# Optimization experiments

Hardware: AMD Instinct MI355X
Metric: run time of the kernel (lower is better)

Reference implementation:

```python
import jax, jax.numpy as jnp
import numpy as np

# Dims from GlobalFractalRouterConfig defaults
B, D, FP, H, NF, A = 65536, 512, 64, 256, 4, 32


def _norm(x):
    # F.normalize(dim=-1) with eps=1e-12
    return x / jnp.clip(jnp.linalg.norm(x, axis=-1, keepdims=True), 1e-12)


def setup_inputs() -> dict:
    key = jax.random.key(0)
    ks = jax.random.split(key, 12)
    s = 0.02
    return {
        "features": jax.random.normal(ks[0], (B, D), jnp.float32),
        "source_fingerprint": jax.random.normal(ks[1], (FP,), jnp.float32),
        "target_fingerprint": jax.random.normal(ks[2], (FP,), jnp.float32),
        # field_generators: NF stacked (Linear(D+FP,H) -> GELU -> Linear(H,1))
        "Wf1": jax.random.normal(ks[3], (NF, D + FP, H), jnp.float32) * s,
        "bf1": jnp.zeros((NF, H), jnp.float32),
        "Wf2": jax.random.normal(ks[4], (NF, H), jnp.float32) * s,
        "bf2": jnp.zeros((NF,), jnp.float32),
        # compat_proj: Linear(2*FP, NF)
        "Wc": jax.random.normal(ks[5], (2 * FP, NF), jnp.float32) * s,
        "bc": jnp.zeros((NF,), jnp.float32),
        # gate_net: Linear(2*NF+FP, H) -> GELU -> Linear(H, D) -> Sigmoid
        "Wg1": jax.random.normal(ks[6], (2 * NF + FP, H), jnp.float32) * s,
        "bg1": jnp.zeros((H,), jnp.float32),
        "Wg2": jax.random.normal(ks[7], (H, D), jnp.float32) * s,
        "bg2": jnp.zeros((D,), jnp.float32),
        # AnchorBank
        "E": jax.random.normal(ks[8], (A, D), jnp.float32) * s,  # anchor_embeddings
        "Wfp": jax.random.normal(ks[9], (D, D), jnp.float32) * s,  # feature_proj
        "bfp": jnp.zeros((D,), jnp.float32),
        "Wfq": jax.random.normal(ks[10], (FP, D), jnp.float32) * s,  # fingerprint_proj
        "bfq": jnp.zeros((D,), jnp.float32),
    }


def _potential(feats, fp_vec, Wf1, bf1, Wf2, bf2):
    # AdjacentGate.compute_potential, all fields vectorized
    b = feats.shape[0]
    comb = jnp.concatenate(
        [feats, jnp.broadcast_to(fp_vec, (b, fp_vec.shape[0]))], axis=-1
    )  # [B, D+FP]
    h = jax.nn.gelu(jnp.einsum('bi,fih->bfh', comb, Wf1) + bf1, approximate=False)
    return jnp.einsum('bfh,fh->bf', h, Wf2) + bf2  # [B, NF]


def reference(features, source_fingerprint, target_fingerprint,
              Wf1, bf1, Wf2, bf2, Wc, bc, Wg1, bg1, Wg2, bg2,
              E, Wfp, bfp, Wfq, bfq):
    b = features.shape[0]
    # --- AdjacentGate ---
    p_src = _potential(features, source_fingerprint, Wf1, bf1, Wf2, bf2)
    p_tgt = _potential(features, target_fingerprint, Wf1, bf1, Wf2, bf2)
    gradient = p_tgt - p_src  # [B, NF]
    fp_comb = jnp.concatenate([source_fingerprint, target_fingerprint])  # [2*FP]
    compat = jnp.tanh(fp_comb @ Wc + bc)  # [NF]
    gate_in = jnp.concatenate(
        [gradient,
         jnp.broadcast_to(compat, (b, compat.shape[0])),
         jnp.broadcast_to(source_fingerprint, (b, source_fingerprint.shape[0]))],
        axis=-1)  # [B, 2*NF+FP]
    gate = jax.nn.sigmoid(
        jax.nn.gelu(gate_in @ Wg1 + bg1, approximate=False) @ Wg2 + bg2)  # [B, D]
    gated = features * gate
    # --- AnchorBank ---
    feat_proj = _norm(gated @ Wfp + bfp)  # [B, D]
    anchors_norm = _norm(E)  # [A, D]
    aff = feat_proj @ anchors_norm.T  # [B, A]
    fp_proj = source_fingerprint @ Wfq + bfq  # [D]
    aff = aff + 0.3 * (anchors_norm @ fp_proj)
    aff = jax.nn.softmax(aff, axis=-1)
    anchor_features = aff @ E  # [B, D]
    return gated + anchor_features
```

## Files before the change

### kernel.cpp

```cpp
#include <hip/hip_runtime.h>
#include <hip/hip_bf16.h>

typedef unsigned short u16;
typedef __attribute__((ext_vector_type(8))) __bf16 bf16x8;
typedef __attribute__((ext_vector_type(8))) short  s16x8;
typedef __attribute__((ext_vector_type(4))) short  s16x4;
typedef __attribute__((ext_vector_type(4))) float  f32x4;

#define NB 65536
#define OFF_GRAD   0u
#define OFF_SUMSQ  1048576u
#define OFF_CONSTS 1310720u
#define OFF_WF1T   1327104u
#define OFF_WG2T   2375680u
#define OFF_WFPT   2637824u
#define OFF_ET     3162112u
#define OFF_AFF    3194880u
#define OFF_GATED  7389184u
#define WS_NEEDED  74498048u
#define CI_SRC   0
#define CI_TGT   1024
#define CI_C0    2048
#define CI_INVE  2304
#define CI_ABIAS 2336

__device__ inline float bf2f(u16 u) { union { unsigned int i; float f; } v; v.i = ((unsigned int)u) << 16; return v.f; }
__device__ inline u16 f2bf(float f) { union { float f; unsigned int i; } v; v.f = f; return (u16)((v.i + 0x7fffu + ((v.i >> 16) & 1u)) >> 16); }
__device__ inline float gelu(float x) {
  float z = 1.5957691216f * x * (1.0f + 0.044715f * x * x);
  return x * __builtin_amdgcn_rcpf(1.0f + __expf(-z));
}
__device__ inline float sigm(float x) { return __builtin_amdgcn_rcpf(1.0f + __expf(-x)); }

typedef __attribute__((address_space(3))) unsigned int as3_u32;
typedef __attribute__((address_space(1))) unsigned int as1_u32;
__device__ __forceinline__ void gload16(const u16* g, u16* l) {
  __builtin_amdgcn_global_load_lds((const as1_u32*)g, (as3_u32*)l, 16, 0, 0);
}

__global__ __launch_bounds__(256) void k_cvt(const float* __restrict__ feat, u16* __restrict__ featbf) {
  int idx = (blockIdx.x << 8) + threadIdx.x;
  const float4* src = (const float4*)feat + (idx << 1);
  float4 v0 = src[0], v1 = src[1];
  s16x8 o;
  o[0] = (short)f2bf(v0.x); o[1] = (short)f2bf(v0.y);
  o[2] = (short)f2bf(v0.z); o[3] = (short)f2bf(v0.w);
  o[4] = (short)f2bf(v1.x); o[5] = (short)f2bf(v1.y);
  o[6] = (short)f2bf(v1.z); o[7] = (short)f2bf(v1.w);
  *(s16x8*)(featbf + (idx << 3)) = o;
}

__global__ __launch_bounds__(256) void k_pre(
    const float* __restrict__ sfp, const float* __restrict__ tfp,
    const float* __restrict__ wf1, const float* __restrict__ bf1,
    const float* __restrict__ wc,  const float* __restrict__ bc,
    const float* __restrict__ wg1, const float* __restrict__ bg1,
    const float* __restrict__ wfq, const float* __restrict__ bfq,
    const float* __restrict__ E,   float* __restrict__ consts)
{
  __shared__ float s_s[64], s_t[64], s_c[4], s_fp[512];
  const int t = threadIdx.x;
  const int b = blockIdx.x;
  if (t < 64) { s_s[t] = sfp[t]; s_t[t] = tfp[t]; }
  __syncthreads();
  if (b < 8) {
    if (t < 128) {
      int n = b * 128 + t;
      int f = n >> 8, h = n & 255;
      float as = bf1[f * 256 + h];
      float at = as;
      const float* col = wf1 + f * 147456 + 512 * 256 + h;
      #pragma unroll 8
      for (int j = 0; j < 64; ++j) {
        float wv = col[j * 256];
        as += s_s[j] * wv; at += s_t[j] * wv;
      }
      consts[CI_SRC + n] = as;
      consts[CI_TGT + n] = at;
    }
  } else if (b == 8) {
    if (t < 4) {
      float a = bc[t];
      for (int j = 0; j < 64; ++j)
        a += s_s[j] * wc[j * 4 + t] + s_t[j] * wc[(64 + j) * 4 + t];
      s_c[t] = tanhf(a);
    }
    __syncthreads();
    float a = bg1[t];
    #pragma unroll
    for (int f = 0; f < 4; ++f) a += s_c[f] * wg1[(4 + f) * 256 + t];
    for (int j = 0; j < 64; ++j) a += s_s[j] * wg1[(8 + j) * 256 + t];
    consts[CI_C0 + t] = a;
  } else {
    for (int d = t; d < 512; d += 256) {
      float a = bfq[d];
      for (int j = 0; j < 64; ++j) a += s_s[j] * wfq[j * 512 + d];
      s_fp[d] = a;
    }
    __syncthreads();
    if (t < 32) {
      float ss = 0.f, dot = 0.f;
      for (int d = 0; d < 512; ++d) {
        float e = E[t * 512 + d];
        ss += e * e; dot += e * s_fp[d];
      }
      float inv = 1.0f / fmaxf(sqrtf(ss), 1e-12f);
      consts[CI_INVE + t] = inv;
      consts[CI_ABIAS + t] = 0.3f * inv * dot;
    }
  }
}

__global__ __launch_bounds__(256) void k_transpose(
    const float* __restrict__ wf1, const float* __restrict__ wg2,
    const float* __restrict__ wfp, const float* __restrict__ E,
    u16* __restrict__ ws16)
{
  int tile = blockIdx.x;
  const float* src; u16* dst; int K, N, tl;
  if (tile < 512)      { int f = tile >> 7; tl = tile & 127; src = wf1 + f * 147456; dst = ws16 + (OFF_WF1T >> 1) + f * 131072; K = 512; N = 256; }
  else if (tile < 640) { tl = tile - 512; src = wg2; dst = ws16 + (OFF_WG2T >> 1); K = 256; N = 512; }
  else if (tile < 896) { tl = tile - 640; src = wfp; dst = ws16 + (OFF_WFPT >> 1); K = 512; N = 512; }
  else                 { tl = tile - 896; src = E;   dst = ws16 + (OFF_ET   >> 1); K = 32;  N = 512; }
  int ntn = N >> 5;
  int r0 = (tl / ntn) << 5, c0 = (tl % ntn) << 5;
  __shared__ float T[32][33];
  const int t = threadIdx.x;
  {
    int r = t >> 3, c4 = (t & 7) << 2;
    float4 v = *(const float4*)(src + (r0 + r) * N + c0 + c4);
    T[r][c4] = v.x; T[r][c4 + 1] = v.y; T[r][c4 + 2] = v.z; T[r][c4 + 3] = v.w;
  }
  __syncthreads();
  {
    int c = t >> 3, r4 = (t & 7) << 2;
    s16x4 v;
    v[0] = (short)f2bf(T[r4 + 0][c]); v[1] = (short)f2bf(T[r4 + 1][c]);
    v[2] = (short)f2bf(T[r4 + 2][c]); v[3] = (short)f2bf(T[r4 + 3][c]);
    *(s16x4*)(dst + (c0 + c) * K + r0 + r4) = v;
  }
}

__global__ __launch_bounds__(256, 2) void k_potential(
    const u16* __restrict__ featbf, const u16* __restrict__ wf1t,
    const float* __restrict__ wf2,  const float* __restrict__ consts,
    float* __restrict__ grad)
{
  __shared__ u16 Al[128][32];
  __shared__ u16 Bl[256][32];
  const int col0 = blockIdx.x << 8;
  const int row0 = blockIdx.y << 7;
  const int f = blockIdx.x;
  const int t = threadIdx.x;
  const int w = t >> 6, lane = t & 63, lr = lane & 15, lq = lane >> 4;
  const int gr = lane >> 2, gc = (lane & 3) << 3;

  f32x4 acc[2][16];
  #pragma unroll
  for (int i = 0; i < 2; ++i)
    #pragma unroll
    for (int j = 0; j < 16; ++j) { f32x4 z = {0.f, 0.f, 0.f, 0.f}; acc[i][j] = z; }

  for (int k0 = 0; k0 < 512; k0 += 32) {
    __syncthreads();
    #pragma unroll
    for (int j = 0; j < 2; ++j) {
      int rb = (j << 6) + (w << 4);
      gload16(featbf + (row0 + rb + gr) * 512 + k0 + gc, &Al[rb][0]);
    }
    #pragma unroll
    for (int j = 0; j < 4; ++j) {
      int rb = (j << 6) + (w << 4);
      gload16(wf1t + (col0 + rb + gr) * 512 + k0 + gc, &Bl[rb][0]);
    }
    __syncthreads();
    bf16x8 a[2];
    #pragma unroll
    for (int rt = 0; rt < 2; ++rt)
      a[rt] = *(const bf16x8*)&Al[(w << 5) + (rt << 4) + lr][lq << 3];
    #pragma unroll
    for (int ct = 0; ct < 16; ++ct) {
      bf16x8 bb = *(const bf16x8*)&Bl[(ct << 4) + lr][lq << 3];
      acc[0][ct] = __builtin_amdgcn_mfma_f32_16x16x32_bf16(a[0], bb, acc[0][ct], 0, 0, 0);
      acc[1][ct] = __builtin_amdgcn_mfma_f32_16x16x32_bf16(a[1], bb, acc[1][ct], 0, 0, 0);
    }
  }
  float part[2][4] = {{0, 0, 0, 0}, {0, 0, 0, 0}};
  #pragma unroll
  for (int ct = 0; ct < 16; ++ct) {
    int n = col0 + (ct << 4) + lr;
    float so = consts[CI_SRC + n];
    float to = consts[CI_TGT + n];
    float w2 = wf2[n];
    #pragma unroll
    for (int rt = 0; rt < 2; ++rt)
      #pragma unroll
      for (int j = 0; j < 4; ++j) {
        float c = acc[rt][ct][j];
        part[rt][j] += (gelu(c + to) - gelu(c + so)) * w2;
      }
  }
  #pragma unroll
  for (int m = 1; m <= 8; m <<= 1)
    #pragma unroll
    for (int rt = 0; rt < 2; ++rt)
      #pragma unroll
      for (int j = 0; j < 4; ++j)
        part[rt][j] += __shfl_xor(part[rt][j], m, 64);
  if (lr == 0) {
    #pragma unroll
    for (int rt = 0; rt < 2; ++rt)
      #pragma unroll
      for (int j = 0; j < 4; ++j) {
        int r = row0 + (w << 5) + (rt << 4) + (lq << 2) + j;
        grad[r * 4 + f] = part[rt][j];
      }
  }
}

__global__ __launch_bounds__(256, 2) void k_gate(
    const u16* __restrict__ featbf, const float* __restrict__ grad,
    const float* __restrict__ wg1,  const u16* __restrict__ wg2t,
    const float* __restrict__ bg2,  const float* __restrict__ consts,
    u16* __restrict__ gated)
{
  __shared__ u16 Hl[128][264];
  __shared__ u16 Bl[128][32];
  const int col0 = blockIdx.x << 7;
  const int row0 = blockIdx.y << 7;
  const int t = threadIdx.x;
  const int w = t >> 6, lane = t & 63, lr = lane & 15, lq = lane >> 4;
  const int gr = lane >> 2, gc = (lane & 3) << 3;

  {
    float wv[4], c0v = consts[CI_C0 + t];
    #pragma unroll
    for (int f = 0; f < 4; ++f) wv[f] = wg1[f * 256 + t];
    for (int i = 0; i < 128; ++i) {
      float4 g = *(const float4*)(grad + ((row0 + i) << 2));
      float p = c0v + g.x * wv[0] + g.y * wv[1] + g.z * wv[2] + g.w * wv[3];
      Hl[i][t] = f2bf(gelu(p));
    }
  }
  f32x4 acc[2][8];
  #pragma unroll
  for (int i = 0; i < 2; ++i)
    #pragma unroll
    for (int j = 0; j < 8; ++j) { f32x4 z = {0.f, 0.f, 0.f, 0.f}; acc[i][j] = z; }

  for (int k0 = 0; k0 < 256; k0 += 32) {
    __syncthreads();
    #pragma unroll
    for (int j = 0; j < 2; ++j) {
      int rb = (j << 6) + (w << 4);
      gload16(wg2t + (col0 + rb + gr) * 256 + k0 + gc, &Bl[rb][0]);
    }
    __syncthreads();
    bf16x8 a[2];
    #pragma unroll
    for (int rt = 0; rt < 2; ++rt)
      a[rt] = *(const bf16x8*)&Hl[(w << 5) + (rt << 4) + lr][k0 + (lq << 3)];
    #pragma unroll
    for (int ct = 0; ct < 8; ++ct) {
      bf16x8 bb = *(const bf16x8*)&Bl[(ct << 4) + lr][lq << 3];
      acc[0][ct] = __builtin_amdgcn_mfma_f32_16x16x32_bf16(a[0], bb, acc[0][ct], 0, 0, 0);
      acc[1][ct] = __builtin_amdgcn_mfma_f32_16x16x32_bf16(a[1], bb, acc[1][ct], 0, 0, 0);
    }
  }
  __syncthreads();
  u16* Gl = &Hl[0][0];
  #pragma unroll
  for (int ct = 0; ct < 8; ++ct) {
    int n = col0 + (ct << 4) + lr;
    float bv = bg2[n];
    #pragma unroll
    for (int rt = 0; rt < 2; ++rt)
      #pragma unroll
      for (int j = 0; j < 4; ++j) {
        int r = (w << 5) + (rt << 4) + (lq << 2) + j;
        Gl[r * 136 + (ct << 4) + lr] = f2bf(sigm(acc[rt][ct][j] + bv));
      }
  }
  __syncthreads();
  #pragma unroll
  for (int it = 0; it < 8; ++it) {
    int s = (it << 8) + t;
    int r = s >> 4, c8 = (s & 15) << 3;
    s16x8 f8 = *(const s16x8*)(featbf + (row0 + r) * 512 + col0 + c8);
    s16x8 g8 = *(const s16x8*)(Gl + r * 136 + c8);
    s16x8 o;
    #pragma unroll
    for (int j = 0; j < 8; ++j)
      o[j] = (short)f2bf(bf2f((u16)f8[j]) * bf2f((u16)g8[j]));
    *(s16x8*)(gated + (row0 + r) * 512 + col0 + c8) = o;
  }
}

__global__ __launch_bounds__(256, 2) void k_proj(
    const u16* __restrict__ gated, const u16* __restrict__ wfpt,
    const float* __restrict__ bfp, u16* __restrict__ y,
    float* __restrict__ sumsq)
{
  __shared__ u16 U[128 * 264];
  u16 (*Al)[32] = (u16(*)[32])U;
  u16 (*Bl)[32] = (u16(*)[32])(U + 4096);
  const int col0 = blockIdx.x << 8;
  const int row0 = blockIdx.y << 7;
  const int t = threadIdx.x;
  const int w = t >> 6, lane = t & 63, lr = lane & 15, lq = lane >> 4;
  const int gr = lane >> 2, gc = (lane & 3) << 3;

  f32x4 acc[2][16];
  #pragma unroll
  for (int i = 0; i < 2; ++i)
    #pragma unroll
    for (int j = 0; j < 16; ++j) { f32x4 z = {0.f, 0.f, 0.f, 0.f}; acc[i][j] = z; }

  for (int k0 = 0; k0 < 512; k0 += 32) {
    __syncthreads();
    #pragma unroll
    for (int j = 0; j < 2; ++j) {
      int rb = (j << 6) + (w << 4);
      gload16(gated + (row0 + rb + gr) * 512 + k0 + gc, &Al[rb][0]);
    }
    #pragma unroll
    for (int j = 0; j < 4; ++j) {
      int rb = (j << 6) + (w << 4);
      gload16(wfpt + (col0 + rb + gr) * 512 + k0 + gc, &Bl[rb][0]);
    }
    __syncthreads();
    bf16x8 a[2];
    #pragma unroll
    for (int rt = 0; rt < 2; ++rt)
      a[rt] = *(const bf16x8*)&Al[(w << 5) + (rt << 4) + lr][lq << 3];
    #pragma unroll
    for (int ct = 0; ct < 16; ++ct) {
      bf16x8 bb = *(const bf16x8*)&Bl[(ct << 4) + lr][lq << 3];
      acc[0][ct] = __builtin_amdgcn_mfma_f32_16x16x32_bf16(a[0], bb, acc[0][ct], 0, 0, 0);
      acc[1][ct] = __builtin_amdgcn_mfma_f32_16x16x32_bf16(a[1], bb, acc[1][ct], 0, 0, 0);
    }
  }
  float part[2][4] = {{0, 0, 0, 0}, {0, 0, 0, 0}};
  #pragma unroll
  for (int ct = 0; ct < 16; ++ct) {
    float bv = bfp[col0 + (ct << 4) + lr];
    #pragma unroll
    for (int rt = 0; rt < 2; ++rt)
      #pragma unroll
      for (int j = 0; j < 4; ++j) {
        acc[rt][ct][j] += bv;
        part[rt][j] += acc[rt][ct][j] * acc[rt][ct][j];
      }
  }
  #pragma unroll
  for (int m = 1; m <= 8; m <<= 1)
    #pragma unroll
    for (int rt = 0; rt < 2; ++rt)
      #pragma unroll
      for (int j = 0; j < 4; ++j)
        part[rt][j] += __shfl_xor(part[rt][j], m, 64);
  if (lr == 0) {
    #pragma unroll
    for (int rt = 0; rt < 2; ++rt)
      #pragma unroll
      for (int j = 0; j < 4; ++j)
        atomicAdd(&sumsq[row0 + (w << 5) + (rt << 4) + (lq << 2) + j], part[rt][j]);
  }
  __syncthreads();
  u16* Yl = U;
  #pragma unroll
  for (int ct = 0; ct < 16; ++ct)
    #pragma unroll
    for (int rt = 0; rt < 2; ++rt)
      #pragma unroll
      for (int j = 0; j < 4; ++j) {
        int r = (w << 5) + (rt << 4) + (lq << 2) + j;
        Yl[r * 264 + (ct << 4) + lr] = f2bf(acc[rt][ct][j]);
      }
  __syncthreads();
  #pragma unroll
  for (int it = 0; it < 16; ++it) {
    int s = (it << 8) + t;
    int r = s >> 5, c8 = (s & 31) << 3;
    *(s16x8*)(y + (row0 + r) * 512 + col0 + c8) = *(const s16x8*)(Yl + r * 264 + c8);
  }
}

__global__ __launch_bounds__(256, 2) void k_aff(
    const u16* __restrict__ y, const float* __restrict__ E,
    const float* __restrict__ sumsq, const float* __restrict__ consts,
    u16* __restrict__ aff)
{
  __shared__ u16 El[32][520];
  __shared__ u16 Al[256][32];
  const int row0 = blockIdx.x << 8;
  const int t = threadIdx.x;
  const int w = t >> 6, lane = t & 63, lr = lane & 15, lq = lane >> 4;
  const int gr = lane >> 2, gc = (lane & 3) << 3;
  #pragma unroll
  for (int i = 0; i < 16; ++i) {
    int s = (i << 8) + t;
    int a = s >> 7, c4 = (s & 127) << 2;
    float4 v = *(const float4*)(E + a * 512 + c4);
    s16x4 b;
    b[0] = (short)f2bf(v.x); b[1] = (short)f2bf(v.y);
    b[2] = (short)f2bf(v.z); b[3] = (short)f2bf(v.w);
    *(s16x4*)&El[a][c4] = b;
  }
  f32x4 acc[4][2];
  #pragma unroll
  for (int i = 0; i < 4; ++i)
    #pragma unroll
    for (int j = 0; j < 2; ++j) { f32x4 z = {0.f, 0.f, 0.f, 0.f}; acc[i][j] = z; }

  for (int k0 = 0; k0 < 512; k0 += 32) {
    __syncthreads();
    #pragma unroll
    for (int j = 0; j < 4; ++j) {
      int rb = (j << 6) + (w << 4);
      gload16(y + (row0 + rb + gr) * 512 + k0 + gc, &Al[rb][0]);
    }
    __syncthreads();
    bf16x8 b0 = *(const bf16x8*)&El[lr][k0 + (lq << 3)];
    bf16x8 b1 = *(const bf16x8*)&El[16 + lr][k0 + (lq << 3)];
    #pragma unroll
    for (int rt = 0; rt < 4; ++rt) {
      bf16x8 a = *(const bf16x8*)&Al[(w << 6) + (rt << 4) + lr][lq << 3];
      acc[rt][0] = __builtin_amdgcn_mfma_f32_16x16x32_bf16(a, b0, acc[rt][0], 0, 0, 0);
      acc[rt][1] = __builtin_amdgcn_mfma_f32_16x16x32_bf16(a, b1, acc[rt][1], 0, 0, 0);
    }
  }
  float iv0 = consts[CI_INVE + lr],  iv1 = consts[CI_INVE + 16 + lr];
  float ab0 = consts[CI_ABIAS + lr], ab1 = consts[CI_ABIAS + 16 + lr];
  #pragma unroll
  for (int rt = 0; rt < 4; ++rt) {
    #pragma unroll
    for (int j = 0; j < 4; ++j) {
      int r = row0 + (w << 6) + (rt << 4) + (lq << 2) + j;
      float invn = 1.0f / fmaxf(sqrtf(sumsq[r]), 1e-12f);
      float v0 = acc[rt][0][j] * iv0 * invn + ab0;
      float v1 = acc[rt][1][j] * iv1 * invn + ab1;
      float mx = fmaxf(v0, v1);
      #pragma unroll
      for (int m = 1; m <= 8; m <<= 1) mx = fmaxf(mx, __shfl_xor(mx, m, 64));
      float e0 = __expf(v0 - mx), e1 = __expf(v1 - mx);
      float sm = e0 + e1;
      #pragma unroll
      for (int m = 1; m <= 8; m <<= 1) sm += __shfl_xor(sm, m, 64);
      float rs = 1.0f / sm;
      aff[r * 32 + lr]      = f2bf(e0 * rs);
      aff[r * 32 + 16 + lr] = f2bf(e1 * rs);
    }
  }
}

__global__ __launch_bounds__(256, 2) void k_out(
    const u16* __restrict__ gated, const u16* __restrict__ aff,
    const u16* __restrict__ et, float* __restrict__ out)
{
  __shared__ u16 ETl[512][40];
  __shared__ u16 Afl[64][40];
  __shared__ u16 Ol[64][520];
  const int row0 = blockIdx.x << 6;
  const int t = threadIdx.x;
  const int w = t >> 6, lane = t & 63, lr = lane & 15, lq = lane >> 4;
  {
    int r = t >> 2, k8 = (t & 3) << 3;
    *(bf16x8*)&Afl[r][k8] = *(const bf16x8*)(aff + (row0 + r) * 32 + k8);
  }
  #pragma unroll
  for (int i = 0; i < 8; ++i) {
    int s = (i << 8) + t;
    int d = s >> 2, k8 = (s & 3) << 3;
    *(bf16x8*)&ETl[d][k8] = *(const bf16x8*)(et + d * 32 + k8);
  }
  __syncthreads();
  bf16x8 a[4];
  #pragma unroll
  for (int rt = 0; rt < 4; ++rt)
    a[rt] = *(const bf16x8*)&Afl[(rt << 4) + lr][lq << 3];
  f32x4 z = {0.f, 0.f, 0.f, 0.f};
  #pragma unroll
  for (int ct = 0; ct < 8; ++ct) {
    bf16x8 bb = *(const bf16x8*)&ETl[(w << 7) + (ct << 4) + lr][lq << 3];
    #pragma unroll
    for (int rt = 0; rt < 4; ++rt) {
      f32x4 o = __builtin_amdgcn_mfma_f32_16x16x32_bf16(a[rt], bb, z, 0, 0, 0);
      #pragma unroll
      for (int j = 0; j < 4; ++j)
        Ol[(rt << 4) + (lq << 2) + j][(w << 7) + (ct << 4) + lr] = f2bf(o[j]);
    }
  }
  __syncthreads();
  #pragma unroll
  for (int it = 0; it < 32; ++it) {
    int s = (it << 8) + t;
    int r = s >> 7, c4 = (s & 127) << 2;
    s16x4 g4 = *(const s16x4*)(gated + (row0 + r) * 512 + c4);
    s16x4 a4 = *(const s16x4*)(&Ol[0][0] + r * 520 + c4);
    float4 o;
    o.x = bf2f((u16)g4[0]) + bf2f((u16)a4[0]);
    o.y = bf2f((u16)g4[1]) + bf2f((u16)a4[1]);
    o.z = bf2f((u16)g4[2]) + bf2f((u16)a4[2]);
    o.w = bf2f((u16)g4[3]) + bf2f((u16)a4[3]);
    *(float4*)(out + (row0 + r) * 512 + c4) = o;
  }
}

extern "C" void kernel_launch(void* const* d_in, const int* in_sizes, int n_in,
                              void* d_out, int out_size, void* d_ws, size_t ws_size,
                              hipStream_t stream) {
  (void)in_sizes; (void)n_in; (void)out_size;
  if (ws_size < WS_NEEDED) return;
  const float* feat = (const float*)d_in[0];
  const float* sfp  = (const float*)d_in[1];
  const float* tfp  = (const float*)d_in[2];
  const float* wf1  = (const float*)d_in[3];
  const float* bf1  = (const float*)d_in[4];
  const float* wf2  = (const float*)d_in[5];
  const float* wc   = (const float*)d_in[7];
  const float* bc   = (const float*)d_in[8];
  const float* wg1  = (const float*)d_in[9];
  const float* bg1  = (const float*)d_in[10];
  const float* wg2  = (const float*)d_in[11];
  const float* bg2  = (const float*)d_in[12];
  const float* E    = (const float*)d_in[13];
  const float* wfp  = (const float*)d_in[14];
  const float* bfp  = (const float*)d_in[15];
  const float* wfq  = (const float*)d_in[16];
  const float* bfq  = (const float*)d_in[17];

  char* ws = (char*)d_ws;
  float* grad   = (float*)(ws + OFF_GRAD);
  float* sumsq  = (float*)(ws + OFF_SUMSQ);
  float* consts = (float*)(ws + OFF_CONSTS);
  u16* ws16  = (u16*)ws;
  u16* wf1t  = (u16*)(ws + OFF_WF1T);
  u16* wg2t  = (u16*)(ws + OFF_WG2T);
  u16* wfpt  = (u16*)(ws + OFF_WFPT);
  u16* et    = (u16*)(ws + OFF_ET);
  u16* aff   = (u16*)(ws + OFF_AFF);
  u16* gated = (u16*)(ws + OFF_GATED);
  u16* yscr  = (u16*)d_out;
  u16* featbf = (u16*)d_out + 33554432;
  float* out = (float*)d_out;

  hipMemsetAsync(ws + OFF_SUMSQ, 0, 262144, stream);
  k_cvt<<<dim3(16384), dim3(256), 0, stream>>>(feat, featbf);
  k_pre<<<dim3(10), dim3(256), 0, stream>>>(sfp, tfp, wf1, bf1, wc, bc, wg1, bg1, wfq, bfq, E, consts);
  k_transpose<<<dim3(912), dim3(256), 0, stream>>>(wf1, wg2, wfp, E, ws16);
  k_potential<<<dim3(4, 512), dim3(256), 0, stream>>>(featbf, wf1t, wf2, consts, grad);
  k_gate<<<dim3(4, 512), dim3(256), 0, stream>>>(featbf, grad, wg1, wg2t, bg2, consts, gated);
  k_proj<<<dim3(2, 512), dim3(256), 0, stream>>>(gated, wfpt, bfp, yscr, sumsq);
  k_aff<<<dim3(256), dim3(256), 0, stream>>>(yscr, E, sumsq, consts, aff);
  k_out<<<dim3(1024), dim3(256), 0, stream>>>(gated, aff, et, out);
}
```

Before: 645.6 us.

## Double-buffer LDS tiles, XOR-swizzle LDS layout, and remap block order in GEMM kernels

Converts the K-loops of the potential, gate, projection and affinity kernels to double-buffered LDS staging, so the next tile's global loads are issued while the current tile is consumed by MFMA. This halves the barriers per K-step. It also applies an XOR swizzle to LDS columns to reduce bank conflicts on the bf16x8 reads. The 2D grids are flattened to 1D with a remapped block order that interleaves blocks, likely for better cache and XCD locality. The cost is extra LDS per block, which may reduce occupancy, plus more complex indexing.

Result: no change. 635.8 us (-1.5%).

```diff
diff --git a/kernel.cpp b/kernel.cpp
--- a/kernel.cpp
+++ b/kernel.cpp
@@ -146,14 +146,18 @@
     const float* __restrict__ wf2,  const float* __restrict__ consts,
     float* __restrict__ grad)
 {
-  __shared__ u16 Al[128][32];
-  __shared__ u16 Bl[256][32];
-  const int col0 = blockIdx.x << 8;
-  const int row0 = blockIdx.y << 7;
-  const int f = blockIdx.x;
+  __shared__ u16 Al[2][128][32];
+  __shared__ u16 Bl[2][256][32];
+  const int wg = blockIdx.x;
+  const int s  = ((wg & 7) << 8) + (wg >> 3);
+  const int f  = s & 3;
+  const int col0 = f << 8;
+  const int row0 = (s >> 2) << 7;
   const int t = threadIdx.x;
   const int w = t >> 6, lane = t & 63, lr = lane & 15, lq = lane >> 4;
-  const int gr = lane >> 2, gc = (lane & 3) << 3;
+  const int gr  = lane >> 2;
+  const int gcs = ((lane & 3) ^ ((lane >> 3) & 3)) << 3;
+  const int ca  = (lq ^ ((lr >> 1) & 3)) << 3;
 
   f32x4 acc[2][16];
   #pragma unroll
@@ -161,30 +165,33 @@
     #pragma unroll
     for (int j = 0; j < 16; ++j) { f32x4 z = {0.f, 0.f, 0.f, 0.f}; acc[i][j] = z; }
 
-  for (int k0 = 0; k0 < 512; k0 += 32) {
-    __syncthreads();
-    #pragma unroll
-    for (int j = 0; j < 2; ++j) {
-      int rb = (j << 6) + (w << 4);
-      gload16(featbf + (row0 + rb + gr) * 512 + k0 + gc, &Al[rb][0]);
-    }
-    #pragma unroll
-    for (int j = 0; j < 4; ++j) {
-      int rb = (j << 6) + (w << 4);
-      gload16(wf1t + (col0 + rb + gr) * 512 + k0 + gc, &Bl[rb][0]);
-    }
-    __syncthreads();
-    bf16x8 a[2];
-    #pragma unroll
-    for (int rt = 0; rt < 2; ++rt)
-      a[rt] = *(const bf16x8*)&Al[(w << 5) + (rt << 4) + lr][lq << 3];
-    #pragma unroll
-    for (int ct = 0; ct < 16; ++ct) {
-      bf16x8 bb = *(const bf16x8*)&Bl[(ct << 4) + lr][lq << 3];
-      acc[0][ct] = __builtin_amdgcn_mfma_f32_16x16x32_bf16(a[0], bb, acc[0][ct], 0, 0, 0);
-      acc[1][ct] = __builtin_amdgcn_mfma_f32_16x16x32_bf16(a[1], bb, acc[1][ct], 0, 0, 0);
-    }
-  }
+#define STAGE_P(buf, k0) { \
+    _Pragma("unroll") for (int j = 0; j < 2; ++j) { int rb = (j << 6) + (w << 4); \
+      gload16(featbf + (row0 + rb + gr) * 512 + (k0) + gcs, &Al[buf][rb][0]); } \
+    _Pragma("unroll") for (int j = 0; j < 4; ++j) { int rb = (j << 6) + (w << 4); \
+      gload16(wf1t + (col0 + rb + gr) * 512 + (k0) + gcs, &Bl[buf][rb][0]); } }
+
+#define COMP_P(buf) { bf16x8 a[2]; \
+    _Pragma("unroll") for (int rt = 0; rt < 2; ++rt) \
+      a[rt] = *(const bf16x8*)&Al[buf][(w << 5) + (rt << 4) + lr][ca]; \
+    _Pragma("unroll") for (int ct = 0; ct < 16; ++ct) { \
+      bf16x8 bb = *(const bf16x8*)&Bl[buf][(ct << 4) + lr][ca]; \
+      acc[0][ct] = __builtin_amdgcn_mfma_f32_16x16x32_bf16(a[0], bb, acc[0][ct], 0, 0, 0); \
+      acc[1][ct] = __builtin_amdgcn_mfma_f32_16x16x32_bf16(a[1], bb, acc[1][ct], 0, 0, 0); } }
+
+  STAGE_P(0, 0);
+  __syncthreads();
+  #pragma unroll
+  for (int k0 = 0; k0 < 512; k0 += 64) {
+    STAGE_P(1, k0 + 32);
+    COMP_P(0);
+    __syncthreads();
+    if (k0 + 64 < 512) STAGE_P(0, k0 + 64);
+    COMP_P(1);
+    __syncthreads();
+  }
+#undef STAGE_P
+#undef COMP_P
   float part[2][4] = {{0, 0, 0, 0}, {0, 0, 0, 0}};
   #pragma unroll
   for (int ct = 0; ct < 16; ++ct) {
@@ -224,22 +231,33 @@
     const float* __restrict__ bg2,  const float* __restrict__ consts,
     u16* __restrict__ gated)
 {
-  __shared__ u16 Hl[128][264];
-  __shared__ u16 Bl[128][32];
-  const int col0 = blockIdx.x << 7;
-  const int row0 = blockIdx.y << 7;
+  __shared__ u16 Hl[32768];
+  __shared__ u16 Bl[2][128][32];
+  const int wg = blockIdx.x;
+  const int s  = ((wg & 7) << 8) + (wg >> 3);
+  const int col0 = (s & 3) << 7;
+  const int row0 = (s >> 2) << 7;
   const int t = threadIdx.x;
   const int w = t >> 6, lane = t & 63, lr = lane & 15, lq = lane >> 4;
-  const int gr = lane >> 2, gc = (lane & 3) << 3;
+  const int gr  = lane >> 2;
+  const int gcs = ((lane & 3) ^ ((lane >> 3) & 3)) << 3;
+  const int ca  = (lq ^ ((lr >> 1) & 3)) << 3;
+
+#define STAGE_G(buf, k0) { \
+    _Pragma("unroll") for (int j = 0; j < 2; ++j) { int rb = (j << 6) + (w << 4); \
+      gload16(wg2t + (col0 + rb + gr) * 256 + (k0) + gcs, &Bl[buf][rb][0]); } }
+
+  STAGE_G(0, 0);
 
   {
     float wv[4], c0v = consts[CI_C0 + t];
+    const int tc = t >> 3, tw = t & 7;
     #pragma unroll
     for (int f = 0; f < 4; ++f) wv[f] = wg1[f * 256 + t];
     for (int i = 0; i < 128; ++i) {
       float4 g = *(const float4*)(grad + ((row0 + i) << 2));
       float p = c0v + g.x * wv[0] + g.y * wv[1] + g.z * wv[2] + g.w * wv[3];
-      Hl[i][t] = f2bf(gelu(p));
+      Hl[i * 256 + ((tc ^ ((i >> 1) & 7)) << 3) + tw] = f2bf(gelu(p));
     }
   }
   f32x4 acc[2][8];
@@ -248,27 +266,29 @@
     #pragma unroll
     for (int j = 0; j < 8; ++j) { f32x4 z = {0.f, 0.f, 0.f, 0.f}; acc[i][j] = z; }
 
-  for (int k0 = 0; k0 < 256; k0 += 32) {
-    __syncthreads();
-    #pragma unroll
-    for (int j = 0; j < 2; ++j) {
-      int rb = (j << 6) + (w << 4);
-      gload16(wg2t + (col0 + rb + gr) * 256 + k0 + gc, &Bl[rb][0]);
-    }
-    __syncthreads();
-    bf16x8 a[2];
-    #pragma unroll
-    for (int rt = 0; rt < 2; ++rt)
-      a[rt] = *(const bf16x8*)&Hl[(w << 5) + (rt << 4) + lr][k0 + (lq << 3)];
-    #pragma unroll
-    for (int ct = 0; ct < 8; ++ct) {
-      bf16x8 bb = *(const bf16x8*)&Bl[(ct << 4) + lr][lq << 3];
-      acc[0][ct] = __builtin_amdgcn_mfma_f32_16x16x32_bf16(a[0], bb, acc[0][ct], 0, 0, 0);
-      acc[1][ct] = __builtin_amdgcn_mfma_f32_16x16x32_bf16(a[1], bb, acc[1][ct], 0, 0, 0);
-    }
-  }
-  __syncthreads();
-  u16* Gl = &Hl[0][0];
+#define COMP_G(buf, k0) { bf16x8 a[2]; \
+    _Pragma("unroll") for (int rt = 0; rt < 2; ++rt) { \
+      int r = (w << 5) + (rt << 4) + lr; \
+      int cq = (((k0) >> 3) + lq) ^ (lr >> 1); \
+      a[rt] = *(const bf16x8*)&Hl[r * 256 + (cq << 3)]; } \
+    _Pragma("unroll") for (int ct = 0; ct < 8; ++ct) { \
+      bf16x8 bb = *(const bf16x8*)&Bl[buf][(ct << 4) + lr][ca]; \
+      acc[0][ct] = __builtin_amdgcn_mfma_f32_16x16x32_bf16(a[0], bb, acc[0][ct], 0, 0, 0); \
+      acc[1][ct] = __builtin_amdgcn_mfma_f32_16x16x32_bf16(a[1], bb, acc[1][ct], 0, 0, 0); } }
+
+  __syncthreads();
+  #pragma unroll
+  for (int k0 = 0; k0 < 256; k0 += 64) {
+    STAGE_G(1, k0 + 32);
+    COMP_G(0, k0);
+    __syncthreads();
+    if (k0 + 64 < 256) STAGE_G(0, k0 + 64);
+    COMP_G(1, k0 + 32);
+    __syncthreads();
+  }
+#undef STAGE_G
+#undef COMP_G
+  u16* Gl = Hl;
   #pragma unroll
   for (int ct = 0; ct < 8; ++ct) {
     int n = col0 + (ct << 4) + lr;
@@ -284,8 +304,8 @@
   __syncthreads();
   #pragma unroll
   for (int it = 0; it < 8; ++it) {
-    int s = (it << 8) + t;
-    int r = s >> 4, c8 = (s & 15) << 3;
+    int s2 = (it << 8) + t;
+    int r = s2 >> 4, c8 = (s2 & 15) << 3;
     s16x8 f8 = *(const s16x8*)(featbf + (row0 + r) * 512 + col0 + c8);
     s16x8 g8 = *(const s16x8*)(Gl + r * 136 + c8);
     s16x8 o;
@@ -301,14 +321,20 @@
     const float* __restrict__ bfp, u16* __restrict__ y,
     float* __restrict__ sumsq)
 {
-  __shared__ u16 U[128 * 264];
-  u16 (*Al)[32] = (u16(*)[32])U;
-  u16 (*Bl)[32] = (u16(*)[32])(U + 4096);
-  const int col0 = blockIdx.x << 8;
-  const int row0 = blockIdx.y << 7;
+  __shared__ u16 U[33792];
+  u16* A0 = U;
+  u16* B0 = U + 4096;
+  u16* A1 = U + 12288;
+  u16* B1 = U + 16384;
+  const int wg = blockIdx.x;
+  const int s  = ((wg & 7) << 7) + (wg >> 3);
+  const int col0 = (s & 1) << 8;
+  const int row0 = (s >> 1) << 7;
   const int t = threadIdx.x;
   const int w = t >> 6, lane = t & 63, lr = lane & 15, lq = lane >> 4;
-  const int gr = lane >> 2, gc = (lane & 3) << 3;
+  const int gr  = lane >> 2;
+  const int gcs = ((lane & 3) ^ ((lane >> 3) & 3)) << 3;
+  const int ca  = (lq ^ ((lr >> 1) & 3)) << 3;
 
   f32x4 acc[2][16];
   #pragma unroll
@@ -316,30 +342,33 @@
     #pragma unroll
     for (int j = 0; j < 16; ++j) { f32x4 z = {0.f, 0.f, 0.f, 0.f}; acc[i][j] = z; }
 
-  for (int k0 = 0; k0 < 512; k0 += 32) {
-    __syncthreads();
-    #pragma unroll
-    for (int j = 0; j < 2; ++j) {
-      int rb = (j << 6) + (w << 4);
-      gload16(gated + (row0 + rb + gr) * 512 + k0 + gc, &Al[rb][0]);
-    }
-    #pragma unroll
-    for (int j = 0; j < 4; ++j) {
-      int rb = (j << 6) + (w << 4);
-      gload16(wfpt + (col0 + rb + gr) * 512 + k0 + gc, &Bl[rb][0]);
-    }
-    __syncthreads();
-    bf16x8 a[2];
-    #pragma unroll
-    for (int rt = 0; rt < 2; ++rt)
-      a[rt] = *(const bf16x8*)&Al[(w << 5) + (rt << 4) + lr][lq << 3];
-    #pragma unroll
-    for (int ct = 0; ct < 16; ++ct) {
-      bf16x8 bb = *(const bf16x8*)&Bl[(ct << 4) + lr][lq << 3];
-      acc[0][ct] = __builtin_amdgcn_mfma_f32_16x16x32_bf16(a[0], bb, acc[0][ct], 0, 0, 0);
-      acc[1][ct] = __builtin_amdgcn_mfma_f32_16x16x32_bf16(a[1], bb, acc[1][ct], 0, 0, 0);
-    }
-  }
+#define STAGE_J(Ab, Bb, k0) { \
+    _Pragma("unroll") for (int j = 0; j < 2; ++j) { int rb = (j << 6) + (w << 4); \
+      gload16(gated + (row0 + rb + gr) * 512 + (k0) + gcs, Ab + rb * 32); } \
+    _Pragma("unroll") for (int j = 0; j < 4; ++j) { int rb = (j << 6) + (w << 4); \
+      gload16(wfpt + (col0 + rb + gr) * 512 + (k0) + gcs, Bb + rb * 32); } }
+
+#define COMP_J(Ab, Bb) { bf16x8 a[2]; \
+    _Pragma("unroll") for (int rt = 0; rt < 2; ++rt) \
+      a[rt] = *(const bf16x8*)&Ab[((w << 5) + (rt << 4) + lr) * 32 + ca]; \
+    _Pragma("unroll") for (int ct = 0; ct < 16; ++ct) { \
+      bf16x8 bb = *(const bf16x8*)&Bb[((ct << 4) + lr) * 32 + ca]; \
+      acc[0][ct] = __builtin_amdgcn_mfma_f32_16x16x32_bf16(a[0], bb, acc[0][ct], 0, 0, 0); \
+      acc[1][ct] = __builtin_amdgcn_mfma_f32_16x16x32_bf16(a[1], bb, acc[1][ct], 0, 0, 0); } }
+
+  STAGE_J(A0, B0, 0);
+  __syncthreads();
+  #pragma unroll
+  for (int k0 = 0; k0 < 512; k0 += 64) {
+    STAGE_J(A1, B1, k0 + 32);
+    COMP_J(A0, B0);
+    __syncthreads();
+    if (k0 + 64 < 512) STAGE_J(A0, B0, k0 + 64);
+    COMP_J(A1, B1);
+    __syncthreads();
+  }
+#undef STAGE_J
+#undef COMP_J
   float part[2][4] = {{0, 0, 0, 0}, {0, 0, 0, 0}};
   #pragma unroll
   for (int ct = 0; ct < 16; ++ct) {
@@ -366,7 +395,6 @@
       for (int j = 0; j < 4; ++j)
         atomicAdd(&sumsq[row0 + (w << 5) + (rt << 4) + (lq << 2) + j], part[rt][j]);
   }
-  __syncthreads();
   u16* Yl = U;
   #pragma unroll
   for (int ct = 0; ct < 16; ++ct)
@@ -380,8 +408,8 @@
   __syncthreads();
   #pragma unroll
   for (int it = 0; it < 16; ++it) {
-    int s = (it << 8) + t;
-    int r = s >> 5, c8 = (s & 31) << 3;
+    int s2 = (it << 8) + t;
+    int r = s2 >> 5, c8 = (s2 & 31) << 3;
     *(s16x8*)(y + (row0 + r) * 512 + col0 + c8) = *(const s16x8*)(Yl + r * 264 + c8);
   }
 }
@@ -392,11 +420,19 @@
     u16* __restrict__ aff)
 {
   __shared__ u16 El[32][520];
-  __shared__ u16 Al[256][32];
+  __shared__ u16 Aa[2][256][32];
   const int row0 = blockIdx.x << 8;
   const int t = threadIdx.x;
   const int w = t >> 6, lane = t & 63, lr = lane & 15, lq = lane >> 4;
-  const int gr = lane >> 2, gc = (lane & 3) << 3;
+  const int gr  = lane >> 2;
+  const int gcs = ((lane & 3) ^ ((lane >> 3) & 3)) << 3;
+  const int ca  = (lq ^ ((lr >> 1) & 3)) << 3;
+
+#define STAGE_A(buf, k0) { \
+    _Pragma("unroll") for (int j = 0; j < 4; ++j) { int rb = (j << 6) + (w << 4); \
+      gload16(y + (row0 + rb + gr) * 512 + (k0) + gcs, &Aa[buf][rb][0]); } }
+
+  STAGE_A(0, 0);
   #pragma unroll
   for (int i = 0; i < 16; ++i) {
     int s = (i << 8) + t;
@@ -413,23 +449,26 @@
     #pragma unroll
     for (int j = 0; j < 2; ++j) { f32x4 z = {0.f, 0.f, 0.f, 0.f}; acc[i][j] = z; }
 
-  for (int k0 = 0; k0 < 512; k0 += 32) {
-    __syncthreads();
-    #pragma unroll
-    for (int j = 0; j < 4; ++j) {
-      int rb = (j << 6) + (w << 4);
-      gload16(y + (row0 + rb + gr) * 512 + k0 + gc, &Al[rb][0]);
-    }
-    __syncthreads();
-    bf16x8 b0 = *(const bf16x8*)&El[lr][k0 + (lq << 3)];
-    bf16x8 b1 = *(const bf16x8*)&El[16 + lr][k0 + (lq << 3)];
-    #pragma unroll
-    for (int rt = 0; rt < 4; ++rt) {
-      bf16x8 a = *(const bf16x8*)&Al[(w << 6) + (rt << 4) + lr][lq << 3];
-      acc[rt][0] = __builtin_amdgcn_mfma_f32_16x16x32_bf16(a, b0, acc[rt][0], 0, 0, 0);
-      acc[rt][1] = __builtin_amdgcn_mfma_f32_16x16x32_bf16(a, b1, acc[rt][1], 0, 0, 0);
-    }
-  }
+#define COMP_A(buf, k0) { \
+    bf16x8 b0 = *(const bf16x8*)&El[lr][(k0) + (lq << 3)]; \
+    bf16x8 b1 = *(const bf16x8*)&El[16 + lr][(k0) + (lq << 3)]; \
+    _Pragma("unroll") for (int rt = 0; rt < 4; ++rt) { \
+      bf16x8 a = *(const bf16x8*)&Aa[buf][(w << 6) + (rt << 4) + lr][ca]; \
+      acc[rt][0] = __builtin_amdgcn_mfma_f32_16x16x32_bf16(a, b0, acc[rt][0], 0, 0, 0); \
+      acc[rt][1] = __builtin_amdgcn_mfma_f32_16x16x32_bf16(a, b1, acc[rt][1], 0, 0, 0); } }
+
+  __syncthreads();
+  #pragma unroll
+  for (int k0 = 0; k0 < 512; k0 += 64) {
+    STAGE_A(1, k0 + 32);
+    COMP_A(0, k0);
+    __syncthreads();
+    if (k0 + 64 < 512) STAGE_A(0, k0 + 64);
+    COMP_A(1, k0 + 32);
+    __syncthreads();
+  }
+#undef STAGE_A
+#undef COMP_A
   float iv0 = consts[CI_INVE + lr],  iv1 = consts[CI_INVE + 16 + lr];
   float ab0 = consts[CI_ABIAS + lr], ab1 = consts[CI_ABIAS + 16 + lr];
   #pragma unroll
@@ -549,9 +588,9 @@
   k_cvt<<<dim3(16384), dim3(256), 0, stream>>>(feat, featbf);
   k_pre<<<dim3(10), dim3(256), 0, stream>>>(sfp, tfp, wf1, bf1, wc, bc, wg1, bg1, wfq, bfq, E, consts);
   k_transpose<<<dim3(912), dim3(256), 0, stream>>>(wf1, wg2, wfp, E, ws16);
-  k_potential<<<dim3(4, 512), dim3(256), 0, stream>>>(featbf, wf1t, wf2, consts, grad);
-  k_gate<<<dim3(4, 512), dim3(256), 0, stream>>>(featbf, grad, wg1, wg2t, bg2, consts, gated);
-  k_proj<<<dim3(2, 512), dim3(256), 0, stream>>>(gated, wfpt, bfp, yscr, sumsq);
+  k_potential<<<dim3(2048), dim3(256), 0, stream>>>(featbf, wf1t, wf2, consts, grad);
+  k_gate<<<dim3(2048), dim3(256), 0, stream>>>(featbf, grad, wg1, wg2t, bg2, consts, gated);
+  k_proj<<<dim3(1024), dim3(256), 0, stream>>>(gated, wfpt, bfp, yscr, sumsq);
   k_aff<<<dim3(256), dim3(256), 0, stream>>>(yscr, E, sumsq, consts, aff);
   k_out<<<dim3(1024), dim3(256), 0, stream>>>(gated, aff, et, out);
 }
```
